# Kernel tuning notes

Measured on AMD Instinct MI355X. Metric: run time of the kernel, lower is better.

The kernel has to match this reference:

```python
import jax, jax.numpy as jnp
import numpy as np

N_NODES = 100000
N_EDGES = 1600000
IN_FEATS = 64
HIDDEN = 64
N_CLASSES = 1


def setup_inputs() -> dict:
    key = jax.random.key(0)
    k0, k1, k2, k3, k4 = jax.random.split(key, 5)
    x = jax.random.normal(k0, (N_NODES, IN_FEATS), dtype=jnp.float32)
    src = jax.random.randint(k1, (N_EDGES,), 0, N_NODES, dtype=jnp.int32)
    dst = jax.random.randint(k2, (N_EDGES,), 0, N_NODES, dtype=jnp.int32)
    W1 = jax.random.normal(k3, (IN_FEATS, HIDDEN), dtype=jnp.float32) * (1.0 / np.sqrt(IN_FEATS))
    b1 = jnp.zeros((HIDDEN,), dtype=jnp.float32)
    W2 = jax.random.normal(k4, (HIDDEN, N_CLASSES), dtype=jnp.float32) * (1.0 / np.sqrt(HIDDEN))
    b2 = jnp.zeros((N_CLASSES,), dtype=jnp.float32)
    return {"x": x, "src": src, "dst": dst, "W1": W1, "b1": b1, "W2": W2, "b2": b2}


def _graph_conv(h, src, dst, W, b, n_nodes):
    # DGL GraphConv, norm='both': D_out^{-1/2} A D_in^{-1/2} h W + b
    ones = jnp.ones(src.shape[0], dtype=h.dtype)
    deg_out = jax.ops.segment_sum(ones, src, num_segments=n_nodes)
    deg_in = jax.ops.segment_sum(ones, dst, num_segments=n_nodes)
    norm_out = jnp.where(deg_out > 0, deg_out, 1.0) ** -0.5  # [N]
    norm_in = jnp.where(deg_in > 0, deg_in, 1.0) ** -0.5
    h = h * norm_out[:, None]
    # project first when it shrinks the message size (matches DGL's in>out path; math identical)
    if W.shape[1] < W.shape[0]:
        h = h @ W
    agg = jax.ops.segment_sum(h[src], dst, num_segments=n_nodes)  # [N, d]
    agg = agg * norm_in[:, None]
    if W.shape[1] >= W.shape[0]:
        agg = agg @ W
    return agg + b


def reference(x, src, dst, W1, b1, W2, b2):
    h = _graph_conv(x, src, dst, W1, b1, N_NODES)
    h = jax.nn.relu(h)
    # dropout p=0.0 -> identity
    h = _graph_conv(h, src, dst, W2, b2, N_NODES)
    return jax.nn.sigmoid(h)
```

## Files before the change

kernel.cpp:

```cpp
#include <hip/hip_runtime.h>

#define NN 100000
#define NE 1600000
#define NW 25000
#define NW4 6250
#define S  64
#define EPS (NE / S)
#define AGG_GRID 2048

typedef unsigned int uint;
typedef _Float16 f16x8 __attribute__((ext_vector_type(8)));
typedef _Float16 f16x2 __attribute__((ext_vector_type(2)));
typedef float f32x4 __attribute__((ext_vector_type(4)));

__global__ void __launch_bounds__(256)
k_hist(const int* __restrict__ src, const int* __restrict__ dst,
       uint* __restrict__ partial_in, uint* __restrict__ partial_out,
       unsigned char* __restrict__ lr) {
    __shared__ uint4 cnt4[NW4];
    uint* cnt = (uint*)cnt4;
    int sl = blockIdx.x;
    int y  = blockIdx.y;
    for (int w = threadIdx.x; w < NW4; w += 256) cnt4[w] = make_uint4(0, 0, 0, 0);
    __syncthreads();
    const int* key = y ? src : dst;
    int base = sl * EPS;
    for (int i4 = threadIdx.x; i4 < EPS / 4; i4 += 256) {
        int e = base + i4 * 4;
        int4 k4 = *(const int4*)&key[e];
        uint sh0 = (uint)(k4.x & 3) * 8u, sh1 = (uint)(k4.y & 3) * 8u;
        uint sh2 = (uint)(k4.z & 3) * 8u, sh3 = (uint)(k4.w & 3) * 8u;
        uint r0 = (atomicAdd(&cnt[k4.x >> 2], 1u << sh0) >> sh0) & 0xffu;
        uint r1 = (atomicAdd(&cnt[k4.y >> 2], 1u << sh1) >> sh1) & 0xffu;
        uint r2 = (atomicAdd(&cnt[k4.z >> 2], 1u << sh2) >> sh2) & 0xffu;
        uint r3 = (atomicAdd(&cnt[k4.w >> 2], 1u << sh3) >> sh3) & 0xffu;
        if (y == 0) {
            uchar4 pk = make_uchar4((unsigned char)r0, (unsigned char)r1,
                                    (unsigned char)r2, (unsigned char)r3);
            *(uchar4*)&lr[e] = pk;
        }
    }
    __syncthreads();
    uint4* dp = (uint4*)((y ? partial_out : partial_in) + (size_t)sl * NW);
    for (int w = threadIdx.x; w < NW4; w += 256) dp[w] = cnt4[w];
}

__global__ void k_degnorm(uint* __restrict__ partial_in, const uint* __restrict__ partial_out,
                          int* __restrict__ deg_in, float* __restrict__ norm_in,
                          float* __restrict__ norm_out, int* __restrict__ bsum) {
    __shared__ int red[4];
    int w = blockIdx.x * 256 + threadIdx.x;
    int mysum = 0;
    if (w < NW) {
        uint run = 0;
#pragma unroll 8
        for (int s = 0; s < S; ++s) {
            uint u = partial_in[(size_t)s * NW + w];
            partial_in[(size_t)s * NW + w] = run;
            run += u;
        }
        uint ro = 0;
#pragma unroll 8
        for (int s = 0; s < S; ++s) ro += partial_out[(size_t)s * NW + w];
        int4 dg;
        float4 fi, fo;
        int d0 = run & 0xff, d1 = (run >> 8) & 0xff, d2 = (run >> 16) & 0xff, d3 = (run >> 24) & 0xff;
        dg = make_int4(d0, d1, d2, d3);
        fi.x = d0 > 0 ? rsqrtf((float)d0) : 1.0f;
        fi.y = d1 > 0 ? rsqrtf((float)d1) : 1.0f;
        fi.z = d2 > 0 ? rsqrtf((float)d2) : 1.0f;
        fi.w = d3 > 0 ? rsqrtf((float)d3) : 1.0f;
        int o0 = ro & 0xff, o1 = (ro >> 8) & 0xff, o2 = (ro >> 16) & 0xff, o3 = (ro >> 24) & 0xff;
        fo.x = o0 > 0 ? rsqrtf((float)o0) : 1.0f;
        fo.y = o1 > 0 ? rsqrtf((float)o1) : 1.0f;
        fo.z = o2 > 0 ? rsqrtf((float)o2) : 1.0f;
        fo.w = o3 > 0 ? rsqrtf((float)o3) : 1.0f;
        *(int4*)&deg_in[w * 4]     = dg;
        *(float4*)&norm_in[w * 4]  = fi;
        *(float4*)&norm_out[w * 4] = fo;
        mysum = d0 + d1 + d2 + d3;
    }
#pragma unroll
    for (int off = 32; off; off >>= 1) mysum += __shfl_xor(mysum, off, 64);
    if ((threadIdx.x & 63) == 0) red[threadIdx.x >> 6] = mysum;
    __syncthreads();
    if (threadIdx.x == 0) bsum[blockIdx.x] = red[0] + red[1] + red[2] + red[3];
}

__global__ void k_bscan(const int* __restrict__ bsum, int* __restrict__ bofs,
                        int* __restrict__ row_ofs, int nb) {
    int lane = threadIdx.x;
    int v0 = (lane * 2     < nb) ? bsum[lane * 2]     : 0;
    int v1 = (lane * 2 + 1 < nb) ? bsum[lane * 2 + 1] : 0;
    int pair = v0 + v1;
    int pre = pair;
#pragma unroll
    for (int off = 1; off < 64; off <<= 1) {
        int u = __shfl_up(pre, off, 64);
        if (lane >= off) pre += u;
    }
    int base = pre - pair;
    if (lane * 2     < nb) bofs[lane * 2]     = base;
    if (lane * 2 + 1 < nb) bofs[lane * 2 + 1] = base + v0;
    if (lane == 63) { bofs[nb] = pre; row_ofs[NN] = pre; }
}

__global__ void k_scan(const int* __restrict__ deg_in, const int* __restrict__ bofs,
                       int* __restrict__ row_ofs) {
    __shared__ int wofs[4];
    int t = threadIdx.x;
    int base = blockIdx.x * 1024 + t * 4;
    int d[4];
#pragma unroll
    for (int k = 0; k < 4; ++k) {
        int n = base + k;
        d[k] = (n < NN) ? deg_in[n] : 0;
    }
    int loc = d[0] + d[1] + d[2] + d[3];
    int v = loc;
    int lane = t & 63;
#pragma unroll
    for (int off = 1; off < 64; off <<= 1) {
        int u = __shfl_up(v, off, 64);
        if (lane >= off) v += u;
    }
    if (lane == 63) wofs[t >> 6] = v;
    __syncthreads();
    int w = t >> 6;
    int wbase = 0;
    if (w > 0) wbase += wofs[0];
    if (w > 1) wbase += wofs[1];
    if (w > 2) wbase += wofs[2];
    int excl = bofs[blockIdx.x] + wbase + (v - loc);
#pragma unroll
    for (int k = 0; k < 4; ++k) {
        int n = base + k;
        if (n < NN) { row_ofs[n] = excl; excl += d[k]; }
    }
}

__global__ void k_replay(const int* __restrict__ src, const int* __restrict__ dst,
                         const uint* __restrict__ base_bytes, const unsigned char* __restrict__ lr,
                         const int* __restrict__ row_ofs, int* __restrict__ csr_src) {
    int e = blockIdx.x * blockDim.x + threadIdx.x;
    if (e < NE) {
        int d  = dst[e];
        int sl = e / EPS;
        uint pw = base_bytes[(size_t)sl * NW + (d >> 2)];
        int b = (int)((pw >> ((d & 3) * 8)) & 0xffu);
        csr_src[row_ofs[d] + b + (int)lr[e]] = src[e];
    }
}

__global__ void __launch_bounds__(256)
k_proj(const float* __restrict__ x, const float* __restrict__ norm_out,
       const float* __restrict__ W1, _Float16* __restrict__ y) {
    int lane = threadIdx.x & 63;
    int col  = lane & 15;
    int kh   = lane >> 4;
    f16x8 wf[4][2];
#pragma unroll
    for (int t = 0; t < 4; ++t)
#pragma unroll
        for (int s = 0; s < 2; ++s)
#pragma unroll
            for (int j = 0; j < 8; ++j)
                wf[t][s][j] = (_Float16)W1[(s * 32 + kh * 8 + j) * 64 + t * 16 + col];
    int tile = blockIdx.x * 4 + (threadIdx.x >> 6);
    if (tile >= NN / 16) return;
    int base = tile * 16;
    int row  = base + col;
    float no = norm_out[row];
    const float* xr = &x[(size_t)row * 64 + kh * 8];
    f16x8 af[2];
#pragma unroll
    for (int s = 0; s < 2; ++s) {
        float4 v0 = *(const float4*)&xr[s * 32];
        float4 v1 = *(const float4*)&xr[s * 32 + 4];
        af[s][0] = (_Float16)(v0.x * no); af[s][1] = (_Float16)(v0.y * no);
        af[s][2] = (_Float16)(v0.z * no); af[s][3] = (_Float16)(v0.w * no);
        af[s][4] = (_Float16)(v1.x * no); af[s][5] = (_Float16)(v1.y * no);
        af[s][6] = (_Float16)(v1.z * no); af[s][7] = (_Float16)(v1.w * no);
    }
    f32x4 acc[4];
#pragma unroll
    for (int t = 0; t < 4; ++t) acc[t] = (f32x4){0.f, 0.f, 0.f, 0.f};
#pragma unroll
    for (int t = 0; t < 4; ++t) {
        acc[t] = __builtin_amdgcn_mfma_f32_16x16x32_f16(af[0], wf[t][0], acc[t], 0, 0, 0);
        acc[t] = __builtin_amdgcn_mfma_f32_16x16x32_f16(af[1], wf[t][1], acc[t], 0, 0, 0);
    }
#pragma unroll
    for (int t = 0; t < 4; ++t)
#pragma unroll
        for (int r = 0; r < 4; ++r)
            y[(size_t)(base + kh * 4 + r) * 64 + t * 16 + col] = (_Float16)acc[t][r];
}

__device__ inline float2 up2(uint u) {
    f16x2 p = __builtin_bit_cast(f16x2, u);
    return make_float2((float)p.x, (float)p.y);
}

__global__ void __launch_bounds__(256)
k_agg1(const int* __restrict__ csr_src, const int* __restrict__ row_ofs,
       const uint* __restrict__ xb, const float* __restrict__ norm_in,
       const float* __restrict__ norm_out,
       const float* __restrict__ b1, const float* __restrict__ W2,
       float* __restrict__ z) {
    int tid = threadIdx.x;
    int lane = tid & 63, q = lane >> 4, lq = lane & 15;
    float4 bb = *(const float4*)&b1[lq * 4];
    float4 ww = *(const float4*)&W2[lq * 4];
    const size_t lqo = (size_t)(lq << 3);
    for (int n = blockIdx.x * 4 + (tid >> 6); n < NN; n += AGG_GRID * 4) {
        int beg = row_ofs[n], end = row_ofs[n + 1];
        float a0 = 0, a1 = 0, a2 = 0, a3 = 0;
        int ei = beg + q;
        for (; ei + 12 < end; ei += 16) {
            int s0 = csr_src[ei], s1 = csr_src[ei + 4];
            int s2 = csr_src[ei + 8], s3 = csr_src[ei + 12];
            uint2 u0 = *(const uint2*)((const char*)xb + ((size_t)s0 << 7) + lqo);
            uint2 u1 = *(const uint2*)((const char*)xb + ((size_t)s1 << 7) + lqo);
            uint2 u2 = *(const uint2*)((const char*)xb + ((size_t)s2 << 7) + lqo);
            uint2 u3 = *(const uint2*)((const char*)xb + ((size_t)s3 << 7) + lqo);
            float2 p0 = up2(u0.x), r0 = up2(u0.y);
            float2 p1 = up2(u1.x), r1 = up2(u1.y);
            float2 p2 = up2(u2.x), r2 = up2(u2.y);
            float2 p3 = up2(u3.x), r3 = up2(u3.y);
            a0 += (p0.x + p1.x) + (p2.x + p3.x);
            a1 += (p0.y + p1.y) + (p2.y + p3.y);
            a2 += (r0.x + r1.x) + (r2.x + r3.x);
            a3 += (r0.y + r1.y) + (r2.y + r3.y);
        }
        for (; ei < end; ei += 4) {
            int s0 = csr_src[ei];
            uint2 u0 = *(const uint2*)((const char*)xb + ((size_t)s0 << 7) + lqo);
            float2 p0 = up2(u0.x), r0 = up2(u0.y);
            a0 += p0.x; a1 += p0.y; a2 += r0.x; a3 += r0.y;
        }
        a0 += __shfl_xor(a0, 16, 64); a0 += __shfl_xor(a0, 32, 64);
        a1 += __shfl_xor(a1, 16, 64); a1 += __shfl_xor(a1, 32, 64);
        a2 += __shfl_xor(a2, 16, 64); a2 += __shfl_xor(a2, 32, 64);
        a3 += __shfl_xor(a3, 16, 64); a3 += __shfl_xor(a3, 32, 64);
        float nin = norm_in[n];
        float h0 = fmaxf(a0 * nin + bb.x, 0.0f);
        float h1 = fmaxf(a1 * nin + bb.y, 0.0f);
        float h2 = fmaxf(a2 * nin + bb.z, 0.0f);
        float h3 = fmaxf(a3 * nin + bb.w, 0.0f);
        float zv = h0 * ww.x + h1 * ww.y + h2 * ww.z + h3 * ww.w;
#pragma unroll
        for (int off = 8; off; off >>= 1) zv += __shfl_xor(zv, off, 64);
        if (lane == 0) z[n] = zv * norm_out[n];
    }
}

__global__ void k_out2(const int* __restrict__ csr_src, const int* __restrict__ row_ofs,
                       const float* __restrict__ z, const float* __restrict__ norm_in,
                       const float* __restrict__ b2, float* __restrict__ out) {
    int n = blockIdx.x * blockDim.x + threadIdx.x;
    if (n < NN) {
        int beg = row_ofs[n], end = row_ofs[n + 1];
        float a = 0.0f;
        int i = beg;
        for (; i + 3 < end; i += 4) {
            float z0 = z[csr_src[i]], z1 = z[csr_src[i + 1]];
            float z2 = z[csr_src[i + 2]], z3 = z[csr_src[i + 3]];
            a += (z0 + z1) + (z2 + z3);
        }
        for (; i < end; ++i) a += z[csr_src[i]];
        float v = a * norm_in[n] + b2[0];
        out[n] = 1.0f / (1.0f + expf(-v));
    }
}


extern "C" void kernel_launch(void* const* d_in, const int* in_sizes, int n_in,
                              void* d_out, int out_size, void* d_ws, size_t ws_size,
                              hipStream_t stream) {
    const float* x   = (const float*)d_in[0];
    const int*   src = (const int*)d_in[1];
    const int*   dst = (const int*)d_in[2];
    const float* W1  = (const float*)d_in[3];
    const float* b1  = (const float*)d_in[4];
    const float* W2  = (const float*)d_in[5];
    const float* b2  = (const float*)d_in[6];
    float* out = (float*)d_out;

    uint* W0 = (uint*)d_ws;
    uint*          partial_in  = W0;
    unsigned char* lr          = (unsigned char*)(W0 + 1600000);
    uint*          partial_out = W0 + 2000000;
    uint*          xb          = W0;
    int*           csr_src     = (int*)(W0 + 3600000);
    int*           row_ofs     = (int*)(W0 + 5200000);
    int*           deg_in      = row_ofs + NN + 32;
    float*         norm_in     = (float*)(deg_in + NN);
    float*         norm_out    = norm_in + NN;
    float*         z           = norm_out + NN;
    int*           bsum        = (int*)(z + NN);
    int*           bofs        = bsum + 128;

    int nb = (NN + 1023) / 1024;

    k_hist   <<<dim3(S, 2), 256, 0, stream>>>(src, dst, partial_in, partial_out, lr);
    k_degnorm<<<nb, 256, 0, stream>>>(partial_in, partial_out, deg_in, norm_in,
                                      norm_out, bsum);
    k_bscan  <<<1, 64, 0, stream>>>(bsum, bofs, row_ofs, nb);
    k_scan   <<<nb, 256, 0, stream>>>(deg_in, bofs, row_ofs);
    k_replay <<<(NE + 255) / 256, 256, 0, stream>>>(src, dst, partial_in, lr, row_ofs, csr_src);

    k_proj   <<<(NN / 16 + 3) / 4, 256, 0, stream>>>(x, norm_out, W1, (_Float16*)xb);
    k_agg1   <<<AGG_GRID, 256, 0, stream>>>(csr_src, row_ofs, xb, norm_in, norm_out,
                                            b1, W2, z);
    k_out2   <<<(NN + 255) / 256, 256, 0, stream>>>(csr_src, row_ofs, z, norm_in, b2, out);
}
```

Before: 133.2 us.

## Split histogram slices asymmetrically and add nontemporal loads on streaming reads

The dst histogram now uses 128 slices while the src histogram keeps 64. The src blocks drop the unused rank extraction, and blocks beyond the src slice count exit early. Nontemporal loads are added for edge arrays, x and csr_src streams so they pollute the cache less. The workspace layout is reshuffled so csr_src aliases partial_out. This relies on partial_out being dead by the time replay writes csr_src, and doubling the dst slices doubles the partial_in scan traffic in degnorm.

```diff
diff --git a/kernel.cpp b/kernel.cpp
--- a/kernel.cpp
+++ b/kernel.cpp
@@ -4,11 +4,14 @@
 #define NE 1600000
 #define NW 25000
 #define NW4 6250
-#define S  64
-#define EPS (NE / S)
+#define S_D 128
+#define EPS_D (NE / S_D)
+#define S_S 64
+#define EPS_S (NE / S_S)
 #define AGG_GRID 2048
 
 typedef unsigned int uint;
+typedef int i32x4 __attribute__((ext_vector_type(4)));
 typedef _Float16 f16x8 __attribute__((ext_vector_type(8)));
 typedef _Float16 f16x2 __attribute__((ext_vector_type(2)));
 typedef float f32x4 __attribute__((ext_vector_type(4)));
@@ -21,28 +24,41 @@
     uint* cnt = (uint*)cnt4;
     int sl = blockIdx.x;
     int y  = blockIdx.y;
+    if (y == 1 && sl >= S_S) return;
     for (int w = threadIdx.x; w < NW4; w += 256) cnt4[w] = make_uint4(0, 0, 0, 0);
     __syncthreads();
-    const int* key = y ? src : dst;
-    int base = sl * EPS;
-    for (int i4 = threadIdx.x; i4 < EPS / 4; i4 += 256) {
-        int e = base + i4 * 4;
-        int4 k4 = *(const int4*)&key[e];
-        uint sh0 = (uint)(k4.x & 3) * 8u, sh1 = (uint)(k4.y & 3) * 8u;
-        uint sh2 = (uint)(k4.z & 3) * 8u, sh3 = (uint)(k4.w & 3) * 8u;
-        uint r0 = (atomicAdd(&cnt[k4.x >> 2], 1u << sh0) >> sh0) & 0xffu;
-        uint r1 = (atomicAdd(&cnt[k4.y >> 2], 1u << sh1) >> sh1) & 0xffu;
-        uint r2 = (atomicAdd(&cnt[k4.z >> 2], 1u << sh2) >> sh2) & 0xffu;
-        uint r3 = (atomicAdd(&cnt[k4.w >> 2], 1u << sh3) >> sh3) & 0xffu;
-        if (y == 0) {
+    if (y == 0) {
+        int base = sl * EPS_D;
+        for (int i4 = threadIdx.x; i4 < EPS_D / 4; i4 += 256) {
+            int e = base + i4 * 4;
+            i32x4 k4 = __builtin_nontemporal_load((const i32x4*)&dst[e]);
+            uint sh0 = (uint)(k4.x & 3) * 8u, sh1 = (uint)(k4.y & 3) * 8u;
+            uint sh2 = (uint)(k4.z & 3) * 8u, sh3 = (uint)(k4.w & 3) * 8u;
+            uint r0 = (atomicAdd(&cnt[k4.x >> 2], 1u << sh0) >> sh0) & 0xffu;
+            uint r1 = (atomicAdd(&cnt[k4.y >> 2], 1u << sh1) >> sh1) & 0xffu;
+            uint r2 = (atomicAdd(&cnt[k4.z >> 2], 1u << sh2) >> sh2) & 0xffu;
+            uint r3 = (atomicAdd(&cnt[k4.w >> 2], 1u << sh3) >> sh3) & 0xffu;
             uchar4 pk = make_uchar4((unsigned char)r0, (unsigned char)r1,
                                     (unsigned char)r2, (unsigned char)r3);
             *(uchar4*)&lr[e] = pk;
         }
-    }
-    __syncthreads();
-    uint4* dp = (uint4*)((y ? partial_out : partial_in) + (size_t)sl * NW);
-    for (int w = threadIdx.x; w < NW4; w += 256) dp[w] = cnt4[w];
+        __syncthreads();
+        uint4* dp = (uint4*)(partial_in + (size_t)sl * NW);
+        for (int w = threadIdx.x; w < NW4; w += 256) dp[w] = cnt4[w];
+    } else {
+        int base = sl * EPS_S;
+        for (int i4 = threadIdx.x; i4 < EPS_S / 4; i4 += 256) {
+            int e = base + i4 * 4;
+            i32x4 k4 = __builtin_nontemporal_load((const i32x4*)&src[e]);
+            atomicAdd(&cnt[k4.x >> 2], 1u << ((uint)(k4.x & 3) * 8u));
+            atomicAdd(&cnt[k4.y >> 2], 1u << ((uint)(k4.y & 3) * 8u));
+            atomicAdd(&cnt[k4.z >> 2], 1u << ((uint)(k4.z & 3) * 8u));
+            atomicAdd(&cnt[k4.w >> 2], 1u << ((uint)(k4.w & 3) * 8u));
+        }
+        __syncthreads();
+        uint4* dp = (uint4*)(partial_out + (size_t)sl * NW);
+        for (int w = threadIdx.x; w < NW4; w += 256) dp[w] = cnt4[w];
+    }
 }
 
 __global__ void k_degnorm(uint* __restrict__ partial_in, const uint* __restrict__ partial_out,
@@ -54,14 +70,14 @@
     if (w < NW) {
         uint run = 0;
 #pragma unroll 8
-        for (int s = 0; s < S; ++s) {
+        for (int s = 0; s < S_D; ++s) {
             uint u = partial_in[(size_t)s * NW + w];
             partial_in[(size_t)s * NW + w] = run;
             run += u;
         }
         uint ro = 0;
 #pragma unroll 8
-        for (int s = 0; s < S; ++s) ro += partial_out[(size_t)s * NW + w];
+        for (int s = 0; s < S_S; ++s) ro += partial_out[(size_t)s * NW + w];
         int4 dg;
         float4 fi, fo;
         int d0 = run & 0xff, d1 = (run >> 8) & 0xff, d2 = (run >> 16) & 0xff, d3 = (run >> 24) & 0xff;
@@ -145,7 +161,7 @@
     int e = blockIdx.x * blockDim.x + threadIdx.x;
     if (e < NE) {
         int d  = dst[e];
-        int sl = e / EPS;
+        int sl = e / EPS_D;
         uint pw = base_bytes[(size_t)sl * NW + (d >> 2)];
         int b = (int)((pw >> ((d & 3) * 8)) & 0xffu);
         csr_src[row_ofs[d] + b + (int)lr[e]] = src[e];
@@ -175,8 +191,8 @@
     f16x8 af[2];
 #pragma unroll
     for (int s = 0; s < 2; ++s) {
-        float4 v0 = *(const float4*)&xr[s * 32];
-        float4 v1 = *(const float4*)&xr[s * 32 + 4];
+        f32x4 v0 = __builtin_nontemporal_load((const f32x4*)&xr[s * 32]);
+        f32x4 v1 = __builtin_nontemporal_load((const f32x4*)&xr[s * 32 + 4]);
         af[s][0] = (_Float16)(v0.x * no); af[s][1] = (_Float16)(v0.y * no);
         af[s][2] = (_Float16)(v0.z * no); af[s][3] = (_Float16)(v0.w * no);
         af[s][4] = (_Float16)(v1.x * no); af[s][5] = (_Float16)(v1.y * no);
@@ -218,8 +234,10 @@
         float a0 = 0, a1 = 0, a2 = 0, a3 = 0;
         int ei = beg + q;
         for (; ei + 12 < end; ei += 16) {
-            int s0 = csr_src[ei], s1 = csr_src[ei + 4];
-            int s2 = csr_src[ei + 8], s3 = csr_src[ei + 12];
+            int s0 = __builtin_nontemporal_load(&csr_src[ei]);
+            int s1 = __builtin_nontemporal_load(&csr_src[ei + 4]);
+            int s2 = __builtin_nontemporal_load(&csr_src[ei + 8]);
+            int s3 = __builtin_nontemporal_load(&csr_src[ei + 12]);
             uint2 u0 = *(const uint2*)((const char*)xb + ((size_t)s0 << 7) + lqo);
             uint2 u1 = *(const uint2*)((const char*)xb + ((size_t)s1 << 7) + lqo);
             uint2 u2 = *(const uint2*)((const char*)xb + ((size_t)s2 << 7) + lqo);
@@ -234,7 +252,7 @@
             a3 += (r0.y + r1.y) + (r2.y + r3.y);
         }
         for (; ei < end; ei += 4) {
-            int s0 = csr_src[ei];
+            int s0 = __builtin_nontemporal_load(&csr_src[ei]);
             uint2 u0 = *(const uint2*)((const char*)xb + ((size_t)s0 << 7) + lqo);
             float2 p0 = up2(u0.x), r0 = up2(u0.y);
             a0 += p0.x; a1 += p0.y; a2 += r0.x; a3 += r0.y;
@@ -264,11 +282,13 @@
         float a = 0.0f;
         int i = beg;
         for (; i + 3 < end; i += 4) {
-            float z0 = z[csr_src[i]], z1 = z[csr_src[i + 1]];
-            float z2 = z[csr_src[i + 2]], z3 = z[csr_src[i + 3]];
-            a += (z0 + z1) + (z2 + z3);
-        }
-        for (; i < end; ++i) a += z[csr_src[i]];
+            int s0 = __builtin_nontemporal_load(&csr_src[i]);
+            int s1 = __builtin_nontemporal_load(&csr_src[i + 1]);
+            int s2 = __builtin_nontemporal_load(&csr_src[i + 2]);
+            int s3 = __builtin_nontemporal_load(&csr_src[i + 3]);
+            a += (z[s0] + z[s1]) + (z[s2] + z[s3]);
+        }
+        for (; i < end; ++i) a += z[__builtin_nontemporal_load(&csr_src[i])];
         float v = a * norm_in[n] + b2[0];
         out[n] = 1.0f / (1.0f + expf(-v));
     }
@@ -289,10 +309,10 @@
 
     uint* W0 = (uint*)d_ws;
     uint*          partial_in  = W0;
-    unsigned char* lr          = (unsigned char*)(W0 + 1600000);
-    uint*          partial_out = W0 + 2000000;
+    uint*          partial_out = W0 + (size_t)S_D * NW;
+    int*           csr_src     = (int*)partial_out;
+    unsigned char* lr          = (unsigned char*)(W0 + 4800000);
     uint*          xb          = W0;
-    int*           csr_src     = (int*)(W0 + 3600000);
     int*           row_ofs     = (int*)(W0 + 5200000);
     int*           deg_in      = row_ofs + NN + 32;
     float*         norm_in     = (float*)(deg_in + NN);
@@ -303,7 +323,7 @@
 
     int nb = (NN + 1023) / 1024;
 
-    k_hist   <<<dim3(S, 2), 256, 0, stream>>>(src, dst, partial_in, partial_out, lr);
+    k_hist   <<<dim3(S_D, 2), 256, 0, stream>>>(src, dst, partial_in, partial_out, lr);
     k_degnorm<<<nb, 256, 0, stream>>>(partial_in, partial_out, deg_in, norm_in,
                                       norm_out, bsum);
     k_bscan  <<<1, 64, 0, stream>>>(bsum, bofs, row_ofs, nb);
```

Measured after the change: 187.5 us. +40.7%, slower.
